# Optimization experiments

Measured on AMD Instinct MI355X. Metric: run time of the kernel, lower is better.

Reference implementation:

```python
import jax, jax.numpy as jnp
import numpy as np

EPS = 1e-5

def _mvn(feat):
    # instance-norm style mean/std over spatial dims; torch .var is unbiased (ddof=1)
    b, c = feat.shape[:2]
    flat = feat.reshape(b, c, -1)
    mu = flat.mean(-1)[:, :, None, None]
    std = jnp.sqrt(flat.var(-1, ddof=1) + EPS)[:, :, None, None]
    return (feat - mu) / std

def setup_inputs() -> dict:
    key = jax.random.key(0)
    ks = jax.random.split(key, 10)
    B, C, H, W = 4, 512, 64, 64
    sc = 0.05
    return {
        "content": jax.random.normal(ks[0], (B, C, H, W), jnp.float32),
        "style": jax.random.normal(ks[1], (B, C, H, W), jnp.float32),
        "content_key": jax.random.normal(ks[2], (B, C, H, W), jnp.float32),
        "style_key": jax.random.normal(ks[3], (B, C, H, W), jnp.float32),
        "Wf": jax.random.normal(ks[4], (C, C), jnp.float32) * sc,
        "bf": jax.random.normal(ks[5], (C,), jnp.float32) * sc,
        "Wg": jax.random.normal(ks[6], (C, C), jnp.float32) * sc,
        "bg": jax.random.normal(ks[7], (C,), jnp.float32) * sc,
        "Wh": jax.random.normal(ks[8], (C, C), jnp.float32) * sc,
        "bh": jax.random.normal(ks[9], (C,), jnp.float32) * sc,
    }

def reference(content, style, content_key, style_key, Wf, bf, Wg, bg, Wh, bh):
    b, C, h, w = content.shape
    hs, ws = style.shape[2], style.shape[3]
    n, m = h * w, hs * ws
    # 1x1 convs are per-pixel linear maps
    Fq = jnp.einsum('oc,bcn->bno', Wf, content_key.reshape(b, -1, n)) + bf      # [b, n, ck]
    G = jnp.einsum('oc,bcn->bon', Wg, style_key.reshape(b, -1, m)) + bg[:, None]  # [b, ck, m]
    V = jnp.einsum('oc,bcn->bno', Wh, style.reshape(b, C, m)) + bh              # [b, m, C]
    S = jax.nn.softmax(jnp.einsum('bnc,bcm->bnm', Fq, G), axis=-1)              # [b, n, m]
    mean = jnp.einsum('bnm,bmc->bnc', S, V)                                     # attention-weighted mean
    m2 = jnp.einsum('bnm,bmc->bnc', S, V * V)                                   # weighted second moment
    std = jnp.sqrt(jax.nn.relu(m2 - mean * mean))
    mean = mean.reshape(b, h, w, C).transpose(0, 3, 1, 2)
    std = std.reshape(b, h, w, C).transpose(0, 3, 1, 2)
    return std * _mvn(content) + mean
```

## Files before the change

### kernel.cpp

```cpp
#include <hip/hip_runtime.h>
#include <math.h>

#define BATCH 4
#define C 512
#define N 4096
#define M 4096
#define MSPLIT 4

typedef __attribute__((ext_vector_type(8))) short short8;
typedef __attribute__((ext_vector_type(8))) __bf16 bf16x8;
typedef __attribute__((ext_vector_type(4))) float f32x4;
typedef __attribute__((ext_vector_type(4))) unsigned int uint4v;

static __device__ __forceinline__ unsigned short f2bf(float x) {
    unsigned u = __float_as_uint(x);
    u += 0x7fff + ((u >> 16) & 1);
    return (unsigned short)(u >> 16);
}
static __device__ __forceinline__ float bf2f(unsigned short h) {
    return __uint_as_float(((unsigned)h) << 16);
}
static __device__ __forceinline__ f32x4 mfma_bf16(short8 a, short8 b, f32x4 c) {
    return __builtin_amdgcn_mfma_f32_16x16x32_bf16(
        __builtin_bit_cast(bf16x8, a), __builtin_bit_cast(bf16x8, b), c, 0, 0, 0);
}
static __device__ __forceinline__ void gload16(const void* g, void* l) {
    __builtin_amdgcn_global_load_lds(
        (const __attribute__((address_space(1))) void*)g,
        (__attribute__((address_space(3))) void*)l, 16, 0, 0);
}
static __device__ __forceinline__ unsigned cvt_pk_bf16(float a, float b) {
    unsigned r;
    asm("v_cvt_pk_bf16_f32 %0, %1, %2" : "=v"(r) : "v"(a), "v"(b));
    return r;
}

__global__ __launch_bounds__(256) void wsplit_kernel(
    const float* __restrict__ W, unsigned short* __restrict__ hi,
    unsigned short* __restrict__ lo)
{
    int i = blockIdx.x * 256 + threadIdx.x;
    float v = W[i];
    unsigned short h = f2bf(v);
    hi[i] = h;
    lo[i] = f2bf(v - bf2f(h));
}

__global__ __launch_bounds__(256) void linear_fg_mfma(
    const float* __restrict__ in,
    const unsigned short* __restrict__ Whi, const unsigned short* __restrict__ Wlo,
    const float* __restrict__ bias,
    unsigned short* __restrict__ out_hi, unsigned short* __restrict__ out_lo)
{
    __shared__ float in_s[32][68];
    __shared__ __align__(16) unsigned short wh_s[64][40];
    __shared__ __align__(16) unsigned short wl_s[64][40];
    const int tid = threadIdx.x;
    const int n0 = blockIdx.x * 64, o0 = blockIdx.y * 64;
    const int w = tid >> 6, lane = tid & 63;
    const int wrow = w >> 1, wcol = w & 1;
    const int lr = lane & 15, q = lane >> 4;
    f32x4 acc[2][2];
    #pragma unroll
    for (int i = 0; i < 2; ++i)
        #pragma unroll
        for (int j = 0; j < 2; ++j) acc[i][j] = (f32x4){0.f, 0.f, 0.f, 0.f};

    for (int kc = 0; kc < C; kc += 32) {
        __syncthreads();
        #pragma unroll
        for (int it = 0; it < 2; ++it) {
            int idx = tid + it * 256;
            int k = idx >> 4, seg = idx & 15;
            *(float4*)&in_s[k][seg * 4] =
                *(const float4*)&in[(size_t)(kc + k) * N + n0 + seg * 4];
        }
        {
            int o = tid >> 2, sg = tid & 3;
            *(float4*)&wh_s[o][sg * 8] = *(const float4*)&Whi[(size_t)(o0 + o) * 512 + kc + sg * 8];
            *(float4*)&wl_s[o][sg * 8] = *(const float4*)&Wlo[(size_t)(o0 + o) * 512 + kc + sg * 8];
        }
        __syncthreads();
        short8 ah[2], al[2], bh[2], bl[2];
        #pragma unroll
        for (int i = 0; i < 2; ++i) {
            int n = wrow * 32 + i * 16 + lr;
            #pragma unroll
            for (int j = 0; j < 8; ++j) {
                float f = in_s[q * 8 + j][n];
                unsigned short h = f2bf(f);
                ah[i][j] = (short)h;
                al[i][j] = (short)f2bf(f - bf2f(h));
            }
        }
        #pragma unroll
        for (int j = 0; j < 2; ++j) {
            int o = wcol * 32 + j * 16 + lr;
            bh[j] = *(const short8*)&wh_s[o][q * 8];
            bl[j] = *(const short8*)&wl_s[o][q * 8];
        }
        #pragma unroll
        for (int i = 0; i < 2; ++i)
            #pragma unroll
            for (int j = 0; j < 2; ++j) {
                acc[i][j] = mfma_bf16(ah[i], bh[j], acc[i][j]);
                acc[i][j] = mfma_bf16(ah[i], bl[j], acc[i][j]);
                acc[i][j] = mfma_bf16(al[i], bh[j], acc[i][j]);
            }
    }
    #pragma unroll
    for (int i = 0; i < 2; ++i)
        #pragma unroll
        for (int j = 0; j < 2; ++j) {
            int o = o0 + wcol * 32 + j * 16 + lr;
            float bo = bias[o];
            #pragma unroll
            for (int r = 0; r < 4; ++r) {
                int n = n0 + wrow * 32 + i * 16 + q * 4 + r;
                float v = acc[i][j][r] + bo;
                unsigned short h = f2bf(v);
                out_hi[(size_t)n * 512 + o] = h;
                out_lo[(size_t)n * 512 + o] = f2bf(v - bf2f(h));
            }
        }
}

__global__ __launch_bounds__(256) void linear_v_mfma(
    const float* __restrict__ in,
    const unsigned short* __restrict__ Whi, const unsigned short* __restrict__ Wlo,
    const float* __restrict__ bias,
    unsigned short* __restrict__ vhT)
{
    __shared__ float in_s[32][68];
    __shared__ __align__(16) unsigned short wh_s[64][40];
    __shared__ __align__(16) unsigned short wl_s[64][40];
    const int tid = threadIdx.x;
    const int m0 = blockIdx.x * 64, o0 = blockIdx.y * 64;
    const int w = tid >> 6, lane = tid & 63;
    const int wrow = w >> 1, wcol = w & 1;
    const int lr = lane & 15, q = lane >> 4;
    f32x4 acc[2][2];
    #pragma unroll
    for (int i = 0; i < 2; ++i)
        #pragma unroll
        for (int j = 0; j < 2; ++j) acc[i][j] = (f32x4){0.f, 0.f, 0.f, 0.f};

    for (int kc = 0; kc < C; kc += 32) {
        __syncthreads();
        #pragma unroll
        for (int it = 0; it < 2; ++it) {
            int idx = tid + it * 256;
            int k = idx >> 4, seg = idx & 15;
            *(float4*)&in_s[k][seg * 4] =
                *(const float4*)&in[(size_t)(kc + k) * N + m0 + seg * 4];
        }
        {
            int o = tid >> 2, sg = tid & 3;
            *(float4*)&wh_s[o][sg * 8] = *(const float4*)&Whi[(size_t)(o0 + o) * 512 + kc + sg * 8];
            *(float4*)&wl_s[o][sg * 8] = *(const float4*)&Wlo[(size_t)(o0 + o) * 512 + kc + sg * 8];
        }
        __syncthreads();
        short8 ah[2], al[2], bh[2], bl[2];
        #pragma unroll
        for (int i = 0; i < 2; ++i) {
            int o = wrow * 32 + i * 16 + lr;
            ah[i] = *(const short8*)&wh_s[o][q * 8];
            al[i] = *(const short8*)&wl_s[o][q * 8];
        }
        #pragma unroll
        for (int j = 0; j < 2; ++j) {
            int m = wcol * 32 + j * 16 + lr;
            #pragma unroll
            for (int t = 0; t < 8; ++t) {
                float f = in_s[q * 8 + t][m];
                unsigned short h = f2bf(f);
                bh[j][t] = (short)h;
                bl[j][t] = (short)f2bf(f - bf2f(h));
            }
        }
        #pragma unroll
        for (int i = 0; i < 2; ++i)
            #pragma unroll
            for (int j = 0; j < 2; ++j) {
                acc[i][j] = mfma_bf16(ah[i], bh[j], acc[i][j]);
                acc[i][j] = mfma_bf16(ah[i], bl[j], acc[i][j]);
                acc[i][j] = mfma_bf16(al[i], bh[j], acc[i][j]);
            }
    }
    #pragma unroll
    for (int i = 0; i < 2; ++i)
        #pragma unroll
        for (int r = 0; r < 4; ++r) {
            int o = o0 + wrow * 32 + i * 16 + q * 4 + r;
            float bo = bias[o];
            #pragma unroll
            for (int j = 0; j < 2; ++j) {
                int m = m0 + wcol * 32 + j * 16 + lr;
                float v = acc[i][j][r] + bo;
                vhT[(size_t)o * M + m] = f2bf(v);
            }
        }
}

__global__ __launch_bounds__(256) void logits_mfma_kernel(
    const unsigned short* __restrict__ Ah, const unsigned short* __restrict__ Al,
    const unsigned short* __restrict__ Bh, const unsigned short* __restrict__ Bl,
    float* __restrict__ S)
{
    __shared__ __align__(16) unsigned short Ah_s[128 * 32];
    __shared__ __align__(16) unsigned short Al_s[128 * 32];
    __shared__ __align__(16) unsigned short Bh_s[128 * 32];
    __shared__ __align__(16) unsigned short Bl_s[128 * 32];
    const int tid = threadIdx.x;
    const int n0 = blockIdx.y * 128, m0 = blockIdx.x * 128;
    const int w = tid >> 6, lane = tid & 63;
    const int wrow = w >> 1, wcol = w & 1;
    const int lr = lane & 15, q = lane >> 4;
    const int srow = lane >> 2, scol = (lane & 3) * 8;
    f32x4 acc[4][4];
    #pragma unroll
    for (int i = 0; i < 4; ++i)
        #pragma unroll
        for (int j = 0; j < 4; ++j)
            acc[i][j] = (f32x4){0.f, 0.f, 0.f, 0.f};

    for (int kc = 0; kc < C; kc += 32) {
        __syncthreads();
        #pragma unroll
        for (int g2 = 0; g2 < 2; ++g2) {
            int g = w * 2 + g2;
            size_t ga = (size_t)(n0 + g * 16 + srow) * C + kc + scol;
            size_t gb = (size_t)(m0 + g * 16 + srow) * C + kc + scol;
            int lo = g * 512;
            gload16(&Ah[ga], &Ah_s[lo]);
            gload16(&Al[ga], &Al_s[lo]);
            gload16(&Bh[gb], &Bh_s[lo]);
            gload16(&Bl[gb], &Bl_s[lo]);
        }
        __syncthreads();
        short8 ah[4], al[4], bh[4], bl[4];
        #pragma unroll
        for (int i = 0; i < 4; ++i) {
            int ro = (wrow * 64 + i * 16 + lr) * 32 + q * 8;
            int co = (wcol * 64 + i * 16 + lr) * 32 + q * 8;
            ah[i] = *(const short8*)&Ah_s[ro];
            al[i] = *(const short8*)&Al_s[ro];
            bh[i] = *(const short8*)&Bh_s[co];
            bl[i] = *(const short8*)&Bl_s[co];
        }
        #pragma unroll
        for (int i = 0; i < 4; ++i)
            #pragma unroll
            for (int j = 0; j < 4; ++j) {
                acc[i][j] = mfma_bf16(ah[i], bh[j], acc[i][j]);
                acc[i][j] = mfma_bf16(ah[i], bl[j], acc[i][j]);
                acc[i][j] = mfma_bf16(al[i], bh[j], acc[i][j]);
            }
    }
    #pragma unroll
    for (int i = 0; i < 4; ++i) {
        int nb = n0 + wrow * 64 + i * 16 + q * 4;
        #pragma unroll
        for (int j = 0; j < 4; ++j) {
            int m = m0 + wcol * 64 + j * 16 + lr;
            #pragma unroll
            for (int r = 0; r < 4; ++r)
                S[(size_t)(nb + r) * M + m] = acc[i][j][r];
        }
    }
}

__global__ __launch_bounds__(256) void rowstat_p_kernel(
    const float* __restrict__ S, unsigned short* __restrict__ P,
    float* __restrict__ rsum)
{
    const int n = blockIdx.x;
    const int tid = threadIdx.x;
    const float* row = S + (size_t)n * M;
    float v[16];
    #pragma unroll
    for (int i = 0; i < 16; ++i) v[i] = row[tid + i * 256];
    float lm = -INFINITY;
    #pragma unroll
    for (int i = 0; i < 16; ++i) lm = fmaxf(lm, v[i]);
    #pragma unroll
    for (int off = 32; off > 0; off >>= 1) lm = fmaxf(lm, __shfl_xor(lm, off, 64));
    __shared__ float red[4];
    __shared__ float redsum[4];
    const int wid = tid >> 6, lane = tid & 63;
    if (lane == 0) red[wid] = lm;
    __syncthreads();
    const float rm = fmaxf(fmaxf(red[0], red[1]), fmaxf(red[2], red[3]));
    float ls = 0.f;
    unsigned short* prow = P + (size_t)n * M;
    #pragma unroll
    for (int i = 0; i < 16; ++i) {
        float p = __expf(v[i] - rm);
        unsigned short pb = f2bf(p);
        prow[tid + i * 256] = pb;
        ls += bf2f(pb);
    }
    #pragma unroll
    for (int off = 32; off > 0; off >>= 1) ls += __shfl_xor(ls, off, 64);
    if (lane == 0) redsum[wid] = ls;
    __syncthreads();
    if (tid == 0) rsum[n] = redsum[0] + redsum[1] + redsum[2] + redsum[3];
}

__global__ __launch_bounds__(256) void apply_partial_kernel(
    const unsigned short* __restrict__ P, const unsigned short* __restrict__ VhT,
    float* __restrict__ accm_p, float* __restrict__ acc2_p)
{
    __shared__ __align__(16) unsigned short P_s[128 * 32];
    __shared__ __align__(16) unsigned short Vh_s[64 * 32];
    const int tid = threadIdx.x;
    const int c0 = blockIdx.x * 64, n0 = blockIdx.y * 128;
    const int z = blockIdx.z;
    const int w = tid >> 6, lane = tid & 63;
    const int wrow = w >> 1, wcol = w & 1;
    const int lr = lane & 15, q = lane >> 4;
    const int srow = lane >> 2, scol = (lane & 3) * 8;
    f32x4 accm[4][2], acc2[4][2];
    #pragma unroll
    for (int i = 0; i < 4; ++i)
        #pragma unroll
        for (int j = 0; j < 2; ++j) {
            accm[i][j] = (f32x4){0.f, 0.f, 0.f, 0.f};
            acc2[i][j] = (f32x4){0.f, 0.f, 0.f, 0.f};
        }

    const int mbeg = z * (M / MSPLIT);
    for (int mc = mbeg; mc < mbeg + M / MSPLIT; mc += 32) {
        __syncthreads();
        #pragma unroll
        for (int g2 = 0; g2 < 2; ++g2) {
            int g = w * 2 + g2;
            gload16(&P[(size_t)(n0 + g * 16 + srow) * M + mc + scol], &P_s[g * 512]);
        }
        gload16(&VhT[(size_t)(c0 + w * 16 + srow) * M + mc + scol], &Vh_s[w * 512]);
        __syncthreads();
        short8 a[4], bh[2], b2h[2], b2l[2];
        #pragma unroll
        for (int i = 0; i < 4; ++i)
            a[i] = *(const short8*)&P_s[(wrow * 64 + i * 16 + lr) * 32 + q * 8];
        #pragma unroll
        for (int j = 0; j < 2; ++j) {
            bh[j] = *(const short8*)&Vh_s[(wcol * 32 + j * 16 + lr) * 32 + q * 8];
            uint4v u = __builtin_bit_cast(uint4v, bh[j]);
            uint4v hv, lv;
            #pragma unroll
            for (int t = 0; t < 4; ++t) {
                float v0 = __uint_as_float(u[t] << 16);
                float v1 = __uint_as_float(u[t] & 0xffff0000u);
                float s0 = v0 * v0, s1 = v1 * v1;
                unsigned hh = cvt_pk_bf16(s0, s1);
                float r0 = s0 - __uint_as_float(hh << 16);
                float r1 = s1 - __uint_as_float(hh & 0xffff0000u);
                hv[t] = hh;
                lv[t] = cvt_pk_bf16(r0, r1);
            }
            b2h[j] = __builtin_bit_cast(short8, hv);
            b2l[j] = __builtin_bit_cast(short8, lv);
        }
        #pragma unroll
        for (int i = 0; i < 4; ++i)
            #pragma unroll
            for (int j = 0; j < 2; ++j) {
                accm[i][j] = mfma_bf16(a[i], bh[j],  accm[i][j]);
                acc2[i][j] = mfma_bf16(a[i], b2h[j], acc2[i][j]);
                acc2[i][j] = mfma_bf16(a[i], b2l[j], acc2[i][j]);
            }
    }
    const size_t pbase = (size_t)z * N * C;
    #pragma unroll
    for (int i = 0; i < 4; ++i) {
        int nb = n0 + wrow * 64 + i * 16 + q * 4;
        #pragma unroll
        for (int j = 0; j < 2; ++j) {
            int c = c0 + wcol * 32 + j * 16 + lr;
            #pragma unroll
            for (int r = 0; r < 4; ++r) {
                size_t off = pbase + (size_t)(nb + r) * C + c;
                accm_p[off] = accm[i][j][r];
                acc2_p[off] = acc2[i][j][r];
            }
        }
    }
}

__global__ __launch_bounds__(256) void combine_kernel(
    const float* __restrict__ accm_p, const float* __restrict__ acc2_p,
    const float* __restrict__ rsum, float* __restrict__ meanw,
    float* __restrict__ stdw)
{
    const size_t idx = ((size_t)blockIdx.x * 256 + threadIdx.x) * 4;
    const int n = (int)(idx >> 9);
    const float inv = 1.0f / rsum[n];
    float sm[4] = {0.f, 0.f, 0.f, 0.f}, s2[4] = {0.f, 0.f, 0.f, 0.f};
    #pragma unroll
    for (int z = 0; z < MSPLIT; ++z) {
        float4 a = *(const float4*)&accm_p[(size_t)z * N * C + idx];
        float4 b = *(const float4*)&acc2_p[(size_t)z * N * C + idx];
        sm[0] += a.x; sm[1] += a.y; sm[2] += a.z; sm[3] += a.w;
        s2[0] += b.x; s2[1] += b.y; s2[2] += b.z; s2[3] += b.w;
    }
    float4 mnv, sdv;
    float* mp = (float*)&mnv;
    float* sp = (float*)&sdv;
    #pragma unroll
    for (int k = 0; k < 4; ++k) {
        float mn = sm[k] * inv;
        float m2 = s2[k] * inv;
        mp[k] = mn;
        sp[k] = sqrtf(fmaxf(m2 - mn * mn, 0.f));
    }
    *(float4*)&meanw[idx] = mnv;
    *(float4*)&stdw[idx]  = sdv;
}

__global__ __launch_bounds__(256) void mvn_kernel(
    const float* __restrict__ content, float* __restrict__ mu, float* __restrict__ rstd)
{
    const int c = blockIdx.x;
    const int tid = threadIdx.x;
    const float* row = content + (size_t)c * N;
    float s = 0.f, ss = 0.f;
    for (int i = tid; i < N; i += 256) {
        float v = row[i];
        s += v;
        ss = fmaf(v, v, ss);
    }
    #pragma unroll
    for (int off = 32; off > 0; off >>= 1) {
        s  += __shfl_xor(s,  off, 64);
        ss += __shfl_xor(ss, off, 64);
    }
    __shared__ float rs[4], rss[4];
    const int wid = tid >> 6, lane = tid & 63;
    if (lane == 0) { rs[wid] = s; rss[wid] = ss; }
    __syncthreads();
    if (tid == 0) {
        float st = rs[0] + rs[1] + rs[2] + rs[3];
        float sst = rss[0] + rss[1] + rss[2] + rss[3];
        float m = st / (float)N;
        float var = (sst - st * st / (float)N) / (float)(N - 1);
        mu[c] = m;
        rstd[c] = rsqrtf(var + 1e-5f);
    }
}

__global__ __launch_bounds__(256) void final_kernel(
    const float* __restrict__ content, const float* __restrict__ meanw,
    const float* __restrict__ stdw, const float* __restrict__ mu,
    const float* __restrict__ rstd, float* __restrict__ out)
{
    __shared__ float mn_s[32][33], sd_s[32][33];
    const int tid = threadIdx.x;
    const int n0 = blockIdx.x * 32;
    const int c0 = blockIdx.y * 32;
    const int tx = tid & 31, ty = tid >> 5;
    #pragma unroll
    for (int i = 0; i < 4; ++i) {
        int n = ty + i * 8;
        mn_s[tx][n] = meanw[(size_t)(n0 + n) * C + c0 + tx];
        sd_s[tx][n] = stdw [(size_t)(n0 + n) * C + c0 + tx];
    }
    __syncthreads();
    #pragma unroll
    for (int i = 0; i < 4; ++i) {
        int c = ty + i * 8;
        float m = mu[c0 + c], r = rstd[c0 + c];
        size_t off = (size_t)(c0 + c) * N + n0 + tx;
        float x = content[off];
        out[off] = sd_s[c][tx] * (x - m) * r + mn_s[c][tx];
    }
}

extern "C" void kernel_launch(void* const* d_in, const int* in_sizes, int n_in,
                              void* d_out, int out_size, void* d_ws, size_t ws_size,
                              hipStream_t stream)
{
    const float* content = (const float*)d_in[0];
    const float* style   = (const float*)d_in[1];
    const float* ckey    = (const float*)d_in[2];
    const float* skey    = (const float*)d_in[3];
    const float* Wf      = (const float*)d_in[4];
    const float* bf      = (const float*)d_in[5];
    const float* Wg      = (const float*)d_in[6];
    const float* bg      = (const float*)d_in[7];
    const float* Wh      = (const float*)d_in[8];
    const float* bh      = (const float*)d_in[9];
    float* out = (float*)d_out;

    const size_t sz_w  = (size_t)512 * 512 * 2;
    const size_t sz_S  = (size_t)N * M * 4;
    const size_t sz_FG = (size_t)N * C * 2;
    const size_t sz_P  = (size_t)N * M * 2;
    const size_t sz_V  = (size_t)C * M * 2;

    char* p = (char*)d_ws;
    auto alloc = [&](size_t bytes) {
        char* r = p;
        p += (bytes + 255) & ~(size_t)255;
        return r;
    };
    unsigned short* WfH = (unsigned short*)alloc(sz_w);
    unsigned short* WfL = (unsigned short*)alloc(sz_w);
    unsigned short* WgH = (unsigned short*)alloc(sz_w);
    unsigned short* WgL = (unsigned short*)alloc(sz_w);
    unsigned short* WhH = (unsigned short*)alloc(sz_w);
    unsigned short* WhL = (unsigned short*)alloc(sz_w);
    float* S = (float*)alloc(sz_S);
    unsigned short* Fh = (unsigned short*)alloc(sz_FG);
    unsigned short* Fl = (unsigned short*)alloc(sz_FG);
    unsigned short* Gh = (unsigned short*)alloc(sz_FG);
    unsigned short* Gl = (unsigned short*)alloc(sz_FG);
    unsigned short* P    = (unsigned short*)alloc(sz_P);
    unsigned short* VhT  = (unsigned short*)alloc(sz_V);
    float* rsum  = (float*)alloc((size_t)N * 4);
    float* meanw = (float*)alloc((size_t)N * C * 4);
    float* stdw  = (float*)alloc((size_t)N * C * 4);
    float* mu    = (float*)alloc((size_t)C * 4);
    float* rstd  = (float*)alloc((size_t)C * 4);

    float* accm_p = S;
    float* acc2_p = S + (size_t)MSPLIT * N * C;

    wsplit_kernel<<<dim3(1024), 256, 0, stream>>>(Wf, WfH, WfL);
    wsplit_kernel<<<dim3(1024), 256, 0, stream>>>(Wg, WgH, WgL);
    wsplit_kernel<<<dim3(1024), 256, 0, stream>>>(Wh, WhH, WhL);

    for (int b = 0; b < BATCH; ++b) {
        const size_t fo = (size_t)b * C * N;
        linear_fg_mfma<<<dim3(N / 64, C / 64), 256, 0, stream>>>(ckey + fo, WfH, WfL, bf, Fh, Fl);
        linear_fg_mfma<<<dim3(M / 64, C / 64), 256, 0, stream>>>(skey + fo, WgH, WgL, bg, Gh, Gl);
        linear_v_mfma<<<dim3(M / 64, C / 64), 256, 0, stream>>>(style + fo, WhH, WhL, bh, VhT);
        logits_mfma_kernel<<<dim3(M / 128, N / 128), 256, 0, stream>>>(Fh, Fl, Gh, Gl, S);
        rowstat_p_kernel<<<dim3(N), 256, 0, stream>>>(S, P, rsum);
        apply_partial_kernel<<<dim3(C / 64, N / 128, MSPLIT), 256, 0, stream>>>(
            P, VhT, accm_p, acc2_p);
        combine_kernel<<<dim3(N * C / 1024), 256, 0, stream>>>(
            accm_p, acc2_p, rsum, meanw, stdw);
        mvn_kernel<<<dim3(C), 256, 0, stream>>>(content + fo, mu, rstd);
        final_kernel<<<dim3(N / 32, C / 32), 256, 0, stream>>>(
            content + fo, meanw, stdw, mu, rstd, out + fo);
    }
}
```

Measured before the change: 1.091 ms.

## Precompute V squared hi/lo splits, widen apply tile to 128 channels, swizzle LDS

The V projection kernel now writes bf16 hi/lo splits of V squared alongside V, so the apply kernel no longer recomputes the squares and their splits on every m-chunk. The apply kernel tile grows from 64 to 128 channels, which halves the grid and the number of times P is reloaded per channel block. P and V are stored with an XOR swizzle on 8-element groups so the LDS fragment reads avoid bank conflicts. In exchange the apply kernel loads three V streams per chunk, the V projection writes three buffers instead of one, and each thread holds twice as many accumulators, which may reduce occupancy.

```diff
diff --git a/kernel.cpp b/kernel.cpp
--- a/kernel.cpp
+++ b/kernel.cpp
@@ -10,7 +10,6 @@
 typedef __attribute__((ext_vector_type(8))) short short8;
 typedef __attribute__((ext_vector_type(8))) __bf16 bf16x8;
 typedef __attribute__((ext_vector_type(4))) float f32x4;
-typedef __attribute__((ext_vector_type(4))) unsigned int uint4v;
 
 static __device__ __forceinline__ unsigned short f2bf(float x) {
     unsigned u = __float_as_uint(x);
@@ -28,11 +27,6 @@
     __builtin_amdgcn_global_load_lds(
         (const __attribute__((address_space(1))) void*)g,
         (__attribute__((address_space(3))) void*)l, 16, 0, 0);
-}
-static __device__ __forceinline__ unsigned cvt_pk_bf16(float a, float b) {
-    unsigned r;
-    asm("v_cvt_pk_bf16_f32 %0, %1, %2" : "=v"(r) : "v"(a), "v"(b));
-    return r;
 }
 
 __global__ __launch_bounds__(256) void wsplit_kernel(
@@ -129,7 +123,8 @@
     const float* __restrict__ in,
     const unsigned short* __restrict__ Whi, const unsigned short* __restrict__ Wlo,
     const float* __restrict__ bias,
-    unsigned short* __restrict__ vhT)
+    unsigned short* __restrict__ vhT, unsigned short* __restrict__ v2hT,
+    unsigned short* __restrict__ v2lT)
 {
     __shared__ float in_s[32][68];
     __shared__ __align__(16) unsigned short wh_s[64][40];
@@ -193,11 +188,20 @@
         for (int r = 0; r < 4; ++r) {
             int o = o0 + wrow * 32 + i * 16 + q * 4 + r;
             float bo = bias[o];
+            const int swz = (o & 3) << 3;
             #pragma unroll
             for (int j = 0; j < 2; ++j) {
                 int m = m0 + wcol * 32 + j * 16 + lr;
                 float v = acc[i][j][r] + bo;
-                vhT[(size_t)o * M + m] = f2bf(v);
+                unsigned short vh = f2bf(v);
+                float vhf = bf2f(vh);
+                float vsq = vhf * vhf;
+                unsigned short v2h = f2bf(vsq);
+                unsigned short v2l = f2bf(vsq - bf2f(v2h));
+                size_t off = (size_t)o * M + (m ^ swz);
+                vhT[off] = vh;
+                v2hT[off] = v2h;
+                v2lT[off] = v2l;
             }
         }
 }
@@ -293,11 +297,12 @@
     const float rm = fmaxf(fmaxf(red[0], red[1]), fmaxf(red[2], red[3]));
     float ls = 0.f;
     unsigned short* prow = P + (size_t)n * M;
+    const int swz = (n & 3) << 3;
     #pragma unroll
     for (int i = 0; i < 16; ++i) {
         float p = __expf(v[i] - rm);
         unsigned short pb = f2bf(p);
-        prow[tid + i * 256] = pb;
+        prow[(tid + i * 256) ^ swz] = pb;
         ls += bf2f(pb);
     }
     #pragma unroll
@@ -309,22 +314,25 @@
 
 __global__ __launch_bounds__(256) void apply_partial_kernel(
     const unsigned short* __restrict__ P, const unsigned short* __restrict__ VhT,
+    const unsigned short* __restrict__ V2hT, const unsigned short* __restrict__ V2lT,
     float* __restrict__ accm_p, float* __restrict__ acc2_p)
 {
     __shared__ __align__(16) unsigned short P_s[128 * 32];
-    __shared__ __align__(16) unsigned short Vh_s[64 * 32];
-    const int tid = threadIdx.x;
-    const int c0 = blockIdx.x * 64, n0 = blockIdx.y * 128;
+    __shared__ __align__(16) unsigned short Vh_s[128 * 32];
+    __shared__ __align__(16) unsigned short V2h_s[128 * 32];
+    __shared__ __align__(16) unsigned short V2l_s[128 * 32];
+    const int tid = threadIdx.x;
+    const int c0 = blockIdx.x * 128, n0 = blockIdx.y * 128;
     const int z = blockIdx.z;
     const int w = tid >> 6, lane = tid & 63;
     const int wrow = w >> 1, wcol = w & 1;
     const int lr = lane & 15, q = lane >> 4;
     const int srow = lane >> 2, scol = (lane & 3) * 8;
-    f32x4 accm[4][2], acc2[4][2];
+    f32x4 accm[4][4], acc2[4][4];
     #pragma unroll
     for (int i = 0; i < 4; ++i)
         #pragma unroll
-        for (int j = 0; j < 2; ++j) {
+        for (int j = 0; j < 4; ++j) {
             accm[i][j] = (f32x4){0.f, 0.f, 0.f, 0.f};
             acc2[i][j] = (f32x4){0.f, 0.f, 0.f, 0.f};
         }
@@ -335,49 +343,43 @@
         #pragma unroll
         for (int g2 = 0; g2 < 2; ++g2) {
             int g = w * 2 + g2;
-            gload16(&P[(size_t)(n0 + g * 16 + srow) * M + mc + scol], &P_s[g * 512]);
-        }
-        gload16(&VhT[(size_t)(c0 + w * 16 + srow) * M + mc + scol], &Vh_s[w * 512]);
-        __syncthreads();
-        short8 a[4], bh[2], b2h[2], b2l[2];
-        #pragma unroll
-        for (int i = 0; i < 4; ++i)
-            a[i] = *(const short8*)&P_s[(wrow * 64 + i * 16 + lr) * 32 + q * 8];
-        #pragma unroll
-        for (int j = 0; j < 2; ++j) {
-            bh[j] = *(const short8*)&Vh_s[(wcol * 32 + j * 16 + lr) * 32 + q * 8];
-            uint4v u = __builtin_bit_cast(uint4v, bh[j]);
-            uint4v hv, lv;
-            #pragma unroll
-            for (int t = 0; t < 4; ++t) {
-                float v0 = __uint_as_float(u[t] << 16);
-                float v1 = __uint_as_float(u[t] & 0xffff0000u);
-                float s0 = v0 * v0, s1 = v1 * v1;
-                unsigned hh = cvt_pk_bf16(s0, s1);
-                float r0 = s0 - __uint_as_float(hh << 16);
-                float r1 = s1 - __uint_as_float(hh & 0xffff0000u);
-                hv[t] = hh;
-                lv[t] = cvt_pk_bf16(r0, r1);
-            }
-            b2h[j] = __builtin_bit_cast(short8, hv);
-            b2l[j] = __builtin_bit_cast(short8, lv);
-        }
-        #pragma unroll
-        for (int i = 0; i < 4; ++i)
-            #pragma unroll
-            for (int j = 0; j < 2; ++j) {
-                accm[i][j] = mfma_bf16(a[i], bh[j],  accm[i][j]);
-                acc2[i][j] = mfma_bf16(a[i], b2h[j], acc2[i][j]);
-                acc2[i][j] = mfma_bf16(a[i], b2l[j], acc2[i][j]);
-            }
+            size_t gp = (size_t)(n0 + g * 16 + srow) * M + mc + scol;
+            size_t gv = (size_t)(c0 + g * 16 + srow) * M + mc + scol;
+            int lo = g * 512;
+            gload16(&P[gp],    &P_s[lo]);
+            gload16(&VhT[gv],  &Vh_s[lo]);
+            gload16(&V2hT[gv], &V2h_s[lo]);
+            gload16(&V2lT[gv], &V2l_s[lo]);
+        }
+        __syncthreads();
+        short8 a[4];
+        #pragma unroll
+        for (int i = 0; i < 4; ++i) {
+            int row = wrow * 64 + i * 16 + lr;
+            a[i] = *(const short8*)&P_s[row * 32 + (q * 8 ^ ((row & 3) << 3))];
+        }
+        #pragma unroll
+        for (int j = 0; j < 4; ++j) {
+            int crow = wcol * 64 + j * 16 + lr;
+            int off = crow * 32 + (q * 8 ^ ((crow & 3) << 3));
+            short8 bh  = *(const short8*)&Vh_s[off];
+            short8 b2h = *(const short8*)&V2h_s[off];
+            short8 b2l = *(const short8*)&V2l_s[off];
+            #pragma unroll
+            for (int i = 0; i < 4; ++i) {
+                accm[i][j] = mfma_bf16(a[i], bh,  accm[i][j]);
+                acc2[i][j] = mfma_bf16(a[i], b2h, acc2[i][j]);
+                acc2[i][j] = mfma_bf16(a[i], b2l, acc2[i][j]);
+            }
+        }
     }
     const size_t pbase = (size_t)z * N * C;
     #pragma unroll
     for (int i = 0; i < 4; ++i) {
         int nb = n0 + wrow * 64 + i * 16 + q * 4;
         #pragma unroll
-        for (int j = 0; j < 2; ++j) {
-            int c = c0 + wcol * 32 + j * 16 + lr;
+        for (int j = 0; j < 4; ++j) {
+            int c = c0 + wcol * 64 + j * 16 + lr;
             #pragma unroll
             for (int r = 0; r < 4; ++r) {
                 size_t off = pbase + (size_t)(nb + r) * C + c;
@@ -517,6 +519,8 @@
     unsigned short* Gl = (unsigned short*)alloc(sz_FG);
     unsigned short* P    = (unsigned short*)alloc(sz_P);
     unsigned short* VhT  = (unsigned short*)alloc(sz_V);
+    unsigned short* V2hT = (unsigned short*)alloc(sz_V);
+    unsigned short* V2lT = (unsigned short*)alloc(sz_V);
     float* rsum  = (float*)alloc((size_t)N * 4);
     float* meanw = (float*)alloc((size_t)N * C * 4);
     float* stdw  = (float*)alloc((size_t)N * C * 4);
@@ -534,11 +538,12 @@
         const size_t fo = (size_t)b * C * N;
         linear_fg_mfma<<<dim3(N / 64, C / 64), 256, 0, stream>>>(ckey + fo, WfH, WfL, bf, Fh, Fl);
         linear_fg_mfma<<<dim3(M / 64, C / 64), 256, 0, stream>>>(skey + fo, WgH, WgL, bg, Gh, Gl);
-        linear_v_mfma<<<dim3(M / 64, C / 64), 256, 0, stream>>>(style + fo, WhH, WhL, bh, VhT);
+        linear_v_mfma<<<dim3(M / 64, C / 64), 256, 0, stream>>>(style + fo, WhH, WhL, bh,
+                                                                VhT, V2hT, V2lT);
         logits_mfma_kernel<<<dim3(M / 128, N / 128), 256, 0, stream>>>(Fh, Fl, Gh, Gl, S);
         rowstat_p_kernel<<<dim3(N), 256, 0, stream>>>(S, P, rsum);
-        apply_partial_kernel<<<dim3(C / 64, N / 128, MSPLIT), 256, 0, stream>>>(
-            P, VhT, accm_p, acc2_p);
+        apply_partial_kernel<<<dim3(C / 128, N / 128, MSPLIT), 256, 0, stream>>>(
+            P, VhT, V2hT, V2lT, accm_p, acc2_p);
         combine_kernel<<<dim3(N * C / 1024), 256, 0, stream>>>(
             accm_p, acc2_p, rsum, meanw, stdw);
         mvn_kernel<<<dim3(C), 256, 0, stream>>>(content + fo, mu, rstd);
```

Result: slower. 1.211 ms (+11.1%).

## Pack split-bf16 operands into K=1536 layout and rewrite logits GEMM with pipelining

Applied to the files above, without the earlier changes.

The F and G projections now write their hi and lo bf16 parts into one interleaved row of width 1536, arranged as [Fh,Fh,Fl] and [Gh,Gl,Gh]. This turns the three-product split-precision logits into a single bf16 GEMM over K=1536. The logits kernel becomes a 256x256-tile, 512-thread kernel with a triple-buffered LDS pipeline, XOR-swizzled shared memory, grouped block swizzling and setprio scheduling. The aim is better MFMA utilisation and more operand reuse, at the cost of extra F/G writes and heavy LDS use that leaves one block per CU.

```diff
diff --git a/kernel.cpp b/kernel.cpp
--- a/kernel.cpp
+++ b/kernel.cpp
@@ -6,6 +6,8 @@
 #define N 4096
 #define M 4096
 #define MSPLIT 4
+#define GK 1536
+#define GNT 48
 
 typedef __attribute__((ext_vector_type(8))) short short8;
 typedef __attribute__((ext_vector_type(8))) __bf16 bf16x8;
@@ -50,7 +52,8 @@
     const float* __restrict__ in,
     const unsigned short* __restrict__ Whi, const unsigned short* __restrict__ Wlo,
     const float* __restrict__ bias,
-    unsigned short* __restrict__ out_hi, unsigned short* __restrict__ out_lo)
+    unsigned short* __restrict__ dstH1, unsigned short* __restrict__ dstH2,
+    unsigned short* __restrict__ dstL)
 {
     __shared__ float in_s[32][68];
     __shared__ __align__(16) unsigned short wh_s[64][40];
@@ -119,8 +122,11 @@
                 int n = n0 + wrow * 32 + i * 16 + q * 4 + r;
                 float v = acc[i][j][r] + bo;
                 unsigned short h = f2bf(v);
-                out_hi[(size_t)n * 512 + o] = h;
-                out_lo[(size_t)n * 512 + o] = f2bf(v - bf2f(h));
+                unsigned short l = f2bf(v - bf2f(h));
+                size_t row = (size_t)n * GK + o;
+                dstH1[row] = h;
+                dstH2[row] = h;
+                dstL[row]  = l;
             }
         }
 }
@@ -202,70 +208,104 @@
         }
 }
 
-__global__ __launch_bounds__(256) void logits_mfma_kernel(
-    const unsigned short* __restrict__ Ah, const unsigned short* __restrict__ Al,
-    const unsigned short* __restrict__ Bh, const unsigned short* __restrict__ Bl,
+__global__ __launch_bounds__(512) void logits_mfma_kernel(
+    const unsigned short* __restrict__ A, const unsigned short* __restrict__ B,
     float* __restrict__ S)
 {
-    __shared__ __align__(16) unsigned short Ah_s[128 * 32];
-    __shared__ __align__(16) unsigned short Al_s[128 * 32];
-    __shared__ __align__(16) unsigned short Bh_s[128 * 32];
-    __shared__ __align__(16) unsigned short Bl_s[128 * 32];
-    const int tid = threadIdx.x;
-    const int n0 = blockIdx.y * 128, m0 = blockIdx.x * 128;
+    __shared__ __align__(16) unsigned short A_s[3][256 * 32];
+    __shared__ __align__(16) unsigned short B_s[3][256 * 32];
+    const int tid = threadIdx.x;
+    const int orig = blockIdx.x;
+    const int sw = (orig & 7) * 32 + (orig >> 3);
+    const int m0 = (sw & 15) * 256, n0 = (sw >> 4) * 256;
     const int w = tid >> 6, lane = tid & 63;
-    const int wrow = w >> 1, wcol = w & 1;
+    const int wm = w >> 2, wn = w & 3;
     const int lr = lane & 15, q = lane >> 4;
-    const int srow = lane >> 2, scol = (lane & 3) * 8;
-    f32x4 acc[4][4];
-    #pragma unroll
-    for (int i = 0; i < 4; ++i)
-        #pragma unroll
-        for (int j = 0; j < 4; ++j)
-            acc[i][j] = (f32x4){0.f, 0.f, 0.f, 0.f};
-
-    for (int kc = 0; kc < C; kc += 32) {
-        __syncthreads();
-        #pragma unroll
-        for (int g2 = 0; g2 < 2; ++g2) {
-            int g = w * 2 + g2;
-            size_t ga = (size_t)(n0 + g * 16 + srow) * C + kc + scol;
-            size_t gb = (size_t)(m0 + g * 16 + srow) * C + kc + scol;
-            int lo = g * 512;
-            gload16(&Ah[ga], &Ah_s[lo]);
-            gload16(&Al[ga], &Al_s[lo]);
-            gload16(&Bh[gb], &Bh_s[lo]);
-            gload16(&Bl[gb], &Bl_s[lo]);
-        }
-        __syncthreads();
-        short8 ah[4], al[4], bh[4], bl[4];
-        #pragma unroll
-        for (int i = 0; i < 4; ++i) {
-            int ro = (wrow * 64 + i * 16 + lr) * 32 + q * 8;
-            int co = (wcol * 64 + i * 16 + lr) * 32 + q * 8;
-            ah[i] = *(const short8*)&Ah_s[ro];
-            al[i] = *(const short8*)&Al_s[ro];
-            bh[i] = *(const short8*)&Bh_s[co];
-            bl[i] = *(const short8*)&Bl_s[co];
-        }
+    const int koff = lr * 32 + ((q ^ ((lr >> 1) & 3)) * 8);
+    const int abase = (wm * 128) * 32 + koff;
+    const int bbase = (wn * 64) * 32 + koff;
+    const int srow_l = lane >> 2;
+    const int schunk = (lane & 3) ^ ((lane >> 3) & 3);
+    size_t gA[2], gB[2];
+    #pragma unroll
+    for (int r = 0; r < 2; ++r) {
+        int trow = w * 32 + r * 16 + srow_l;
+        gA[r] = (size_t)(n0 + trow) * GK + (size_t)schunk * 8;
+        gB[r] = (size_t)(m0 + trow) * GK + (size_t)schunk * 8;
+    }
+
+    f32x4 acc[8][4];
+    #pragma unroll
+    for (int i = 0; i < 8; ++i)
+        #pragma unroll
+        for (int j = 0; j < 4; ++j) acc[i][j] = (f32x4){0.f, 0.f, 0.f, 0.f};
+
+    #define STAGE_A(buf, t)                                            \
+        { _Pragma("unroll")                                            \
+          for (int r = 0; r < 2; ++r)                                  \
+              gload16(A + gA[r] + (size_t)(t) * 32,                    \
+                      &A_s[buf][(w * 2 + r) * 512]); }
+    #define STAGE_B(buf, t)                                            \
+        { _Pragma("unroll")                                            \
+          for (int r = 0; r < 2; ++r)                                  \
+              gload16(B + gB[r] + (size_t)(t) * 32,                    \
+                      &B_s[buf][(w * 2 + r) * 512]); }
+
+    STAGE_A(0, 0); STAGE_B(0, 0);
+    STAGE_A(1, 1); STAGE_B(1, 1);
+
+    int bc = 0;
+    for (int t = 0; t < GNT; ++t) {
+        if (t < GNT - 1) asm volatile("s_waitcnt vmcnt(4)" ::: "memory");
+        else             asm volatile("s_waitcnt vmcnt(0)" ::: "memory");
+        __builtin_amdgcn_s_barrier();
+        __builtin_amdgcn_sched_barrier(0);
+        const unsigned short* As = A_s[bc];
+        const unsigned short* Bs = B_s[bc];
+        int bn = bc + 2; if (bn >= 3) bn -= 3;
+        short8 bfr[4], afr[4];
+        #pragma unroll
+        for (int j = 0; j < 4; ++j) bfr[j] = *(const short8*)&Bs[bbase + j * 512];
+        #pragma unroll
+        for (int i = 0; i < 4; ++i) afr[i] = *(const short8*)&As[abase + i * 512];
+        if (t + 2 < GNT) STAGE_A(bn, t + 2);
+        __builtin_amdgcn_s_barrier();
+        __builtin_amdgcn_sched_barrier(0);
+        __builtin_amdgcn_s_setprio(1);
         #pragma unroll
         for (int i = 0; i < 4; ++i)
             #pragma unroll
-            for (int j = 0; j < 4; ++j) {
-                acc[i][j] = mfma_bf16(ah[i], bh[j], acc[i][j]);
-                acc[i][j] = mfma_bf16(ah[i], bl[j], acc[i][j]);
-                acc[i][j] = mfma_bf16(al[i], bh[j], acc[i][j]);
-            }
-    }
-    #pragma unroll
-    for (int i = 0; i < 4; ++i) {
-        int nb = n0 + wrow * 64 + i * 16 + q * 4;
+            for (int j = 0; j < 4; ++j)
+                acc[i][j] = mfma_bf16(afr[i], bfr[j], acc[i][j]);
+        __builtin_amdgcn_s_setprio(0);
+        __builtin_amdgcn_s_barrier();
+        __builtin_amdgcn_sched_barrier(0);
+        #pragma unroll
+        for (int i = 0; i < 4; ++i) afr[i] = *(const short8*)&As[abase + (i + 4) * 512];
+        if (t + 2 < GNT) STAGE_B(bn, t + 2);
+        __builtin_amdgcn_s_barrier();
+        __builtin_amdgcn_sched_barrier(0);
+        __builtin_amdgcn_s_setprio(1);
+        #pragma unroll
+        for (int i = 0; i < 4; ++i)
+            #pragma unroll
+            for (int j = 0; j < 4; ++j)
+                acc[i + 4][j] = mfma_bf16(afr[i], bfr[j], acc[i + 4][j]);
+        __builtin_amdgcn_s_setprio(0);
+        bc += 1; if (bc >= 3) bc -= 3;
+    }
+    #undef STAGE_A
+    #undef STAGE_B
+
+    #pragma unroll
+    for (int i = 0; i < 8; ++i) {
+        int n = n0 + wm * 128 + i * 16 + q * 4;
         #pragma unroll
         for (int j = 0; j < 4; ++j) {
-            int m = m0 + wcol * 64 + j * 16 + lr;
+            int m = m0 + wn * 64 + j * 16 + lr;
             #pragma unroll
             for (int r = 0; r < 4; ++r)
-                S[(size_t)(nb + r) * M + m] = acc[i][j][r];
+                S[(size_t)(n + r) * M + m] = acc[i][j][r];
         }
     }
 }
@@ -494,7 +534,7 @@
 
     const size_t sz_w  = (size_t)512 * 512 * 2;
     const size_t sz_S  = (size_t)N * M * 4;
-    const size_t sz_FG = (size_t)N * C * 2;
+    const size_t sz_FG = (size_t)N * GK * 2;
     const size_t sz_P  = (size_t)N * M * 2;
     const size_t sz_V  = (size_t)C * M * 2;
 
@@ -511,10 +551,8 @@
     unsigned short* WhH = (unsigned short*)alloc(sz_w);
     unsigned short* WhL = (unsigned short*)alloc(sz_w);
     float* S = (float*)alloc(sz_S);
-    unsigned short* Fh = (unsigned short*)alloc(sz_FG);
-    unsigned short* Fl = (unsigned short*)alloc(sz_FG);
-    unsigned short* Gh = (unsigned short*)alloc(sz_FG);
-    unsigned short* Gl = (unsigned short*)alloc(sz_FG);
+    unsigned short* Fp = (unsigned short*)alloc(sz_FG);
+    unsigned short* Gp = (unsigned short*)alloc(sz_FG);
     unsigned short* P    = (unsigned short*)alloc(sz_P);
     unsigned short* VhT  = (unsigned short*)alloc(sz_V);
     float* rsum  = (float*)alloc((size_t)N * 4);
@@ -532,10 +570,13 @@
 
     for (int b = 0; b < BATCH; ++b) {
         const size_t fo = (size_t)b * C * N;
-        linear_fg_mfma<<<dim3(N / 64, C / 64), 256, 0, stream>>>(ckey + fo, WfH, WfL, bf, Fh, Fl);
-        linear_fg_mfma<<<dim3(M / 64, C / 64), 256, 0, stream>>>(skey + fo, WgH, WgL, bg, Gh, Gl);
-        linear_v_mfma<<<dim3(M / 64, C / 64), 256, 0, stream>>>(style + fo, WhH, WhL, bh, VhT);
-        logits_mfma_kernel<<<dim3(M / 128, N / 128), 256, 0, stream>>>(Fh, Fl, Gh, Gl, S);
+        linear_fg_mfma<<<dim3(N / 64, C / 64), 256, 0, stream>>>(
+            ckey + fo, WfH, WfL, bf, Fp, Fp + 512, Fp + 1024);
+        linear_fg_mfma<<<dim3(M / 64, C / 64), 256, 0, stream>>>(
+            skey + fo, WgH, WgL, bg, Gp, Gp + 1024, Gp + 512);
+        linear_v_mfma<<<dim3(M / 64, C / 64), 256, 0, stream>>>(
+            style + fo, WhH, WhL, bh, VhT);
+        logits_mfma_kernel<<<dim3(256), 512, 0, stream>>>(Fp, Gp, S);
         rowstat_p_kernel<<<dim3(N), 256, 0, stream>>>(S, P, rsum);
         apply_partial_kernel<<<dim3(C / 64, N / 128, MSPLIT), 256, 0, stream>>>(
             P, VhT, accm_p, acc2_p);
```

Result: slower. 1.116 ms (+2.3%).
